# Performance work log

Hardware: AMD Instinct MI355X
Metric: run time of the kernel (lower is better)

The kernel has to match this reference:

```python
import jax, jax.numpy as jnp
import numpy as np
from jax import lax

ITER, L, D, H = 8, 4096, 512, 256


def setup_inputs() -> dict:
    key = jax.random.key(0)
    ks = jax.random.split(key, 12)
    sD = 1.0 / np.sqrt(D)
    sH = 1.0 / np.sqrt(H)
    return {
        "embeddings_seq": jax.random.normal(ks[0], (ITER, L, D), jnp.float32),
        "ROIs": jax.random.uniform(ks[1], (1, L, 3), jnp.float32),
        "Wx": jax.random.normal(ks[2], (L, D), jnp.float32) * sD,
        "bx": jax.random.normal(ks[3], (L,), jnp.float32) * 0.01,
        "Wy": jax.random.normal(ks[4], (L, D), jnp.float32) * sD,
        "by": jax.random.normal(ks[5], (L,), jnp.float32) * 0.01,
        "Wz": jax.random.normal(ks[6], (L, D), jnp.float32) * sD,
        "bz": jax.random.normal(ks[7], (L,), jnp.float32) * 0.01,
        "Ws": jax.random.normal(ks[8], (D, H), jnp.float32) * sD,
        "bs": jax.random.normal(ks[9], (H,), jnp.float32) * 0.01,
        "Wh": jax.random.normal(ks[10], (L, H), jnp.float32) * sH,
        "bh": jax.random.normal(ks[11], (L,), jnp.float32) * 0.01,
    }


def reference(embeddings_seq, ROIs, Wx, bx, Wy, by, Wz, bz, Ws, bs, Wh, bh):
    # size_tensor = [1/767, 1/767, 1/575]
    size = jnp.array([1.0 / 767, 1.0 / 767, 1.0 / 575], dtype=embeddings_seq.dtype)

    def dec(h):  # grouped Conv1d(k=D, groups=L) == per-landmark dot product; h: [L, D]
        x = jnp.sum(Wx * h, axis=-1) + bx
        y = jnp.sum(Wy * h, axis=-1) + by
        z = jnp.sum(Wz * h, axis=-1) + bz
        return jnp.stack([x, y, z], axis=-1)  # [L, 3]

    def gate_head(h):  # Linear+Tanh shared, then per-landmark grouped conv; h: [L, D]
        s = jnp.tanh(h @ Ws + bs)          # [L, H]
        return jnp.sum(Wh * s, axis=-1) + bh  # [L]

    emb0 = embeddings_seq[0]                  # [L, D]
    rois0 = ROIs[0]                           # [L, 3]
    predict0 = dec(emb0) * size + rois0       # [L, 3]

    def step(carry, emb):
        h, c, pred = carry
        rois = pred                           # previous prediction becomes new ROIs
        gf = gate_head(h)                     # [L]
        ga = gate_head(emb)                   # [L]
        g = jax.nn.softmax(jnp.stack([gf, ga], axis=-1), axis=-1)  # [L, 2]
        g0, g1 = g[:, 0:1], g[:, 1:2]
        h = h * g0 + emb * g1
        c = c * g0 + rois * g1
        pred = dec(h) * size + lax.stop_gradient(c)
        return (h, c, pred), pred

    init = (emb0, rois0, predict0)
    _, preds = lax.scan(step, init, embeddings_seq[1:])  # [ITER-1, L, 3]
    return jnp.concatenate([predict0[None], preds], axis=0)  # [ITER, L, 3]
```

## Files before the change

kernel.cpp:

```cpp
#include <hip/hip_runtime.h>
#include <stdint.h>

#define L_DIM 4096
#define D_DIM 512
#define H_DIM 256
#define T_DIM 8

typedef short bf16x8 __attribute__((ext_vector_type(8)));
typedef float f32x4 __attribute__((ext_vector_type(4)));

__device__ __forceinline__ unsigned short f2bf(float f) {
    union { float f; unsigned int u; } c; c.f = f;
    unsigned int u = c.u;
    unsigned int r = (u + 0x7fffu + ((u >> 16) & 1u)) >> 16;
    return (unsigned short)r;
}

__device__ __forceinline__ float wave_sum(float x) {
    #pragma unroll
    for (int off = 32; off > 0; off >>= 1) x += __shfl_xor(x, off, 64);
    return x;
}

__device__ __forceinline__ float dot4(float4 a, float4 b) {
    return a.x * b.x + a.y * b.y + a.z * b.z + a.w * b.w;
}

__device__ __forceinline__ float fast_tanh(float x) {
    float e = __expf(2.0f * x);
    return 1.0f - 2.0f / (e + 1.0f);
}

__global__ void k_transpose_ws(const float* __restrict__ Ws,
                               unsigned short* __restrict__ WsT) {
    int idx = blockIdx.x * 256 + threadIdx.x;
    int j = idx >> 9;
    int k = idx & 511;
    WsT[idx] = f2bf(Ws[k * H_DIM + j]);
}

__global__ __launch_bounds__(512) void k_gemm_v(const float* __restrict__ emb,
                                                const unsigned short* __restrict__ WsT,
                                                float* __restrict__ v) {
    __shared__ __align__(16) char smem[48 * 1024];
    char* As = smem;
    char* Bs = smem + 16 * 1024;

    const int tid  = threadIdx.x;
    const int lane = tid & 63;
    const int wid  = tid >> 6;
    const int wm   = wid & 1;
    const int wn   = wid >> 1;
    const long rowBase = (long)blockIdx.x * 128;

    f32x4 zero = {0.f, 0.f, 0.f, 0.f};
    f32x4 acc[4][4];
    #pragma unroll
    for (int mi = 0; mi < 4; mi++)
        #pragma unroll
        for (int ni = 0; ni < 4; ni++) acc[mi][ni] = zero;

    for (int kt = 0; kt < 8; ++kt) {
        __syncthreads();
        #pragma unroll
        for (int p = 0; p < 4; p++) {
            int g   = p * 512 + tid;
            int row = g >> 4;
            int q   = g & 15;
            float4 s = *(const float4*)(emb + (rowBase + row) * D_DIM + kt * 64 + q * 4);
            unsigned short b0 = f2bf(s.x), b1 = f2bf(s.y), b2 = f2bf(s.z), b3 = f2bf(s.w);
            uint2 pk;
            pk.x = (unsigned int)b0 | ((unsigned int)b1 << 16);
            pk.y = (unsigned int)b2 | ((unsigned int)b3 << 16);
            *(uint2*)(As + (row * 128 + ((q * 8) ^ ((row & 7) << 4)))) = pk;
        }
        #pragma unroll
        for (int p = 0; p < 4; p++) {
            int g  = p * 512 + tid;
            int j  = g >> 3;
            int ko = g & 7;
            uint4 d = *(const uint4*)(WsT + j * D_DIM + kt * 64 + ko * 8);
            *(uint4*)(Bs + (j * 128 + ((ko * 16) ^ ((j & 7) << 4)))) = d;
        }
        __syncthreads();

        #pragma unroll
        for (int ks = 0; ks < 2; ++ks) {
            bf16x8 a[4], b[4];
            #pragma unroll
            for (int mi = 0; mi < 4; mi++) {
                int row = wm * 64 + mi * 16 + (lane & 15);
                a[mi] = *(const bf16x8*)(As + (row * 128 +
                          ((ks * 64 + (lane >> 4) * 16) ^ ((row & 7) << 4))));
            }
            #pragma unroll
            for (int ni = 0; ni < 4; ni++) {
                int j = wn * 64 + ni * 16 + (lane & 15);
                b[ni] = *(const bf16x8*)(Bs + (j * 128 +
                          ((ks * 64 + (lane >> 4) * 16) ^ ((j & 7) << 4))));
            }
            #pragma unroll
            for (int mi = 0; mi < 4; mi++)
                #pragma unroll
                for (int ni = 0; ni < 4; ni++)
                    acc[mi][ni] = __builtin_amdgcn_mfma_f32_16x16x32_bf16(
                        a[mi], b[ni], acc[mi][ni], 0, 0, 0);
        }
    }

    #pragma unroll
    for (int mi = 0; mi < 4; mi++)
        #pragma unroll
        for (int ni = 0; ni < 4; ni++)
            #pragma unroll
            for (int r = 0; r < 4; r++) {
                long row = rowBase + wm * 64 + mi * 16 + (lane >> 4) * 4 + r;
                int  col = wn * 64 + ni * 16 + (lane & 15);
                v[row * H_DIM + col] = acc[mi][ni][r];
            }
}

__global__ __launch_bounds__(256) void k_seq(
    const float* __restrict__ emb, const float* __restrict__ rois,
    const float* __restrict__ Wx, const float* __restrict__ bx,
    const float* __restrict__ Wy, const float* __restrict__ by,
    const float* __restrict__ Wz, const float* __restrict__ bz,
    const float* __restrict__ bs, const float* __restrict__ Wh,
    const float* __restrict__ bh, const float* __restrict__ v,
    float* __restrict__ out) {
    const int lane = threadIdx.x & 63;
    const int l = blockIdx.x * 4 + (threadIdx.x >> 6);
    const int j4 = lane * 4;
    const int d8 = lane * 8;

    float4 Wh4 = *(const float4*)(Wh + (long)l * H_DIM + j4);
    float4 bs4 = *(const float4*)(bs + j4);
    float4 wx0 = *(const float4*)(Wx + (long)l * D_DIM + d8);
    float4 wx1 = *(const float4*)(Wx + (long)l * D_DIM + d8 + 4);
    float4 wy0 = *(const float4*)(Wy + (long)l * D_DIM + d8);
    float4 wy1 = *(const float4*)(Wy + (long)l * D_DIM + d8 + 4);
    float4 wz0 = *(const float4*)(Wz + (long)l * D_DIM + d8);
    float4 wz1 = *(const float4*)(Wz + (long)l * D_DIM + d8 + 4);
    float bxl = bx[l], byl = by[l], bzl = bz[l], bhl = bh[l];
    const float sx = 1.f / 767.f, sy = 1.f / 767.f, sz = 1.f / 575.f;

    float4 e0 = *(const float4*)(emb + (long)l * D_DIM + d8);
    float4 e1 = *(const float4*)(emb + (long)l * D_DIM + d8 + 4);
    float dx = wave_sum(dot4(wx0, e0) + dot4(wx1, e1));
    float dy = wave_sum(dot4(wy0, e0) + dot4(wy1, e1));
    float dz = wave_sum(dot4(wz0, e0) + dot4(wz1, e1));
    float4 u4 = *(const float4*)(v + (long)l * H_DIM + j4);
    float cx = rois[l * 3 + 0], cy = rois[l * 3 + 1], cz = rois[l * 3 + 2];
    float prx = (dx + bxl) * sx + cx;
    float pry = (dy + byl) * sy + cy;
    float prz = (dz + bzl) * sz + cz;
    if (lane == 0) {
        out[l * 3 + 0] = prx; out[l * 3 + 1] = pry; out[l * 3 + 2] = prz;
    }

    for (int t = 1; t < T_DIM; ++t) {
        const float* eb = emb + ((long)t * L_DIM + l) * D_DIM;
        float4 f0 = *(const float4*)(eb + d8);
        float4 f1 = *(const float4*)(eb + d8 + 4);
        float4 v4 = *(const float4*)(v + ((long)t * L_DIM + l) * H_DIM + j4);

        float pxt = wave_sum(dot4(wx0, f0) + dot4(wx1, f1));
        float pyt = wave_sum(dot4(wy0, f0) + dot4(wy1, f1));
        float pzt = wave_sum(dot4(wz0, f0) + dot4(wz1, f1));

        float4 sf, sa;
        sf.x = fast_tanh(u4.x + bs4.x); sf.y = fast_tanh(u4.y + bs4.y);
        sf.z = fast_tanh(u4.z + bs4.z); sf.w = fast_tanh(u4.w + bs4.w);
        sa.x = fast_tanh(v4.x + bs4.x); sa.y = fast_tanh(v4.y + bs4.y);
        sa.z = fast_tanh(v4.z + bs4.z); sa.w = fast_tanh(v4.w + bs4.w);
        float gf = wave_sum(dot4(Wh4, sf)) + bhl;
        float ga = wave_sum(dot4(Wh4, sa)) + bhl;

        float g0 = 1.0f / (1.0f + __expf(ga - gf));
        float g1 = 1.0f - g0;

        u4.x = g0 * u4.x + g1 * v4.x; u4.y = g0 * u4.y + g1 * v4.y;
        u4.z = g0 * u4.z + g1 * v4.z; u4.w = g0 * u4.w + g1 * v4.w;

        cx = cx * g0 + prx * g1; cy = cy * g0 + pry * g1; cz = cz * g0 + prz * g1;
        dx = g0 * dx + g1 * pxt; dy = g0 * dy + g1 * pyt; dz = g0 * dz + g1 * pzt;

        prx = (dx + bxl) * sx + cx;
        pry = (dy + byl) * sy + cy;
        prz = (dz + bzl) * sz + cz;
        if (lane == 0) {
            float* o = out + (long)t * (L_DIM * 3) + l * 3;
            o[0] = prx; o[1] = pry; o[2] = prz;
        }
    }
}

extern "C" void kernel_launch(void* const* d_in, const int* in_sizes, int n_in,
                              void* d_out, int out_size, void* d_ws, size_t ws_size,
                              hipStream_t stream) {
    const float* emb  = (const float*)d_in[0];
    const float* rois = (const float*)d_in[1];
    const float* Wx   = (const float*)d_in[2];
    const float* bx   = (const float*)d_in[3];
    const float* Wy   = (const float*)d_in[4];
    const float* by   = (const float*)d_in[5];
    const float* Wz   = (const float*)d_in[6];
    const float* bz   = (const float*)d_in[7];
    const float* Ws   = (const float*)d_in[8];
    const float* bs   = (const float*)d_in[9];
    const float* Wh   = (const float*)d_in[10];
    const float* bh   = (const float*)d_in[11];
    float* out = (float*)d_out;

    float* v = (float*)d_ws;
    unsigned short* WsT = (unsigned short*)((char*)d_ws + (size_t)32768 * 256 * 4);

    hipLaunchKernelGGL(k_transpose_ws, dim3(512), dim3(256), 0, stream, Ws, WsT);
    hipLaunchKernelGGL(k_gemm_v, dim3(256), dim3(512), 0, stream, emb, WsT, v);
    hipLaunchKernelGGL(k_seq, dim3(1024), dim3(256), 0, stream,
                       emb, rois, Wx, bx, Wy, by, Wz, bz, bs, Wh, bh, v, out);
}
```

Before: 163.9 us.

## Double-buffer GEMM tiles, store v in bf16, batch independent reductions in seq kernel

The GEMM kernel now uses 64-row tiles over 512 blocks, with double-buffered shared memory so the next K slice is fetched from global memory while MFMAs run on the current one. It writes v as bf16 instead of fp32, halving the intermediate write and read traffic. The sequential kernel now loads all timesteps up front and does their independent dot products, tanh and wave reductions before the recurrence, leaving only the forget-gate reduction on the serial path. The costs are extra rounding of v to bf16, more registers, and 80 KB of shared memory per block, which limits occupancy.

```diff
diff --git a/kernel.cpp b/kernel.cpp
--- a/kernel.cpp
+++ b/kernel.cpp
@@ -16,6 +16,19 @@
     return (unsigned short)r;
 }
 
+__device__ __forceinline__ float bits2f(unsigned int u) {
+    union { unsigned int u; float f; } c; c.u = u; return c.f;
+}
+
+__device__ __forceinline__ float4 unpack_bf4(uint2 q) {
+    float4 r;
+    r.x = bits2f(q.x << 16);
+    r.y = bits2f(q.x & 0xffff0000u);
+    r.z = bits2f(q.y << 16);
+    r.w = bits2f(q.y & 0xffff0000u);
+    return r;
+}
+
 __device__ __forceinline__ float wave_sum(float x) {
     #pragma unroll
     for (int off = 32; off > 0; off >>= 1) x += __shfl_xor(x, off, 64);
@@ -29,6 +42,13 @@
 __device__ __forceinline__ float fast_tanh(float x) {
     float e = __expf(2.0f * x);
     return 1.0f - 2.0f / (e + 1.0f);
+}
+
+__device__ __forceinline__ float4 tanh4b(float4 a, float4 b) {
+    float4 r;
+    r.x = fast_tanh(a.x + b.x); r.y = fast_tanh(a.y + b.y);
+    r.z = fast_tanh(a.z + b.z); r.w = fast_tanh(a.w + b.w);
+    return r;
 }
 
 __global__ void k_transpose_ws(const float* __restrict__ Ws,
@@ -39,84 +59,124 @@
     WsT[idx] = f2bf(Ws[k * H_DIM + j]);
 }
 
-__global__ __launch_bounds__(512) void k_gemm_v(const float* __restrict__ emb,
-                                                const unsigned short* __restrict__ WsT,
-                                                float* __restrict__ v) {
-    __shared__ __align__(16) char smem[48 * 1024];
-    char* As = smem;
-    char* Bs = smem + 16 * 1024;
+__global__ __launch_bounds__(512, 4) void k_gemm_v(
+    const float* __restrict__ emb,
+    const unsigned short* __restrict__ WsT,
+    unsigned short* __restrict__ v) {
+    __shared__ __align__(16) char smem[81920];
 
     const int tid  = threadIdx.x;
     const int lane = tid & 63;
     const int wid  = tid >> 6;
-    const int wm   = wid & 1;
-    const int wn   = wid >> 1;
-    const long rowBase = (long)blockIdx.x * 128;
-
-    f32x4 zero = {0.f, 0.f, 0.f, 0.f};
-    f32x4 acc[4][4];
-    #pragma unroll
-    for (int mi = 0; mi < 4; mi++)
-        #pragma unroll
-        for (int ni = 0; ni < 4; ni++) acc[mi][ni] = zero;
-
+    const int wm   = wid >> 2;
+    const int wn   = wid & 3;
+    const long rowBase = (long)blockIdx.x * 64;
+
+    const int arow = tid >> 4, aq = tid & 15;
+    const int bj   = tid >> 3, bko = tid & 7;
+    const float*          ag = emb + (rowBase + arow) * D_DIM + aq * 4;
+    const unsigned short* bg = WsT + (long)bj * D_DIM + bko * 8;
+
+    const int adst0 = arow * 128 + ((aq * 8) ^ ((arow & 7) << 4));
+    const int adst1 = (arow + 32) * 128 + ((aq * 8) ^ (((arow + 32) & 7) << 4));
+    const int bdst[4] = {
+        bj * 128 + ((bko * 16) ^ ((bj & 7) << 4)),
+        (bj + 64) * 128 + ((bko * 16) ^ (((bj + 64) & 7) << 4)),
+        (bj + 128) * 128 + ((bko * 16) ^ (((bj + 128) & 7) << 4)),
+        (bj + 192) * 128 + ((bko * 16) ^ (((bj + 192) & 7) << 4))};
+
+    f32x4 acc[2][4];
+    #pragma unroll
+    for (int mi = 0; mi < 2; mi++)
+        #pragma unroll
+        for (int ni = 0; ni < 4; ni++) acc[mi][ni] = (f32x4){0.f, 0.f, 0.f, 0.f};
+
+    {
+        float4 a0 = *(const float4*)(ag);
+        float4 a1 = *(const float4*)(ag + 32 * D_DIM);
+        char* As = smem;
+        char* Bs = smem + 8192;
+        uint2 p0, p1;
+        p0.x = (unsigned)f2bf(a0.x) | ((unsigned)f2bf(a0.y) << 16);
+        p0.y = (unsigned)f2bf(a0.z) | ((unsigned)f2bf(a0.w) << 16);
+        p1.x = (unsigned)f2bf(a1.x) | ((unsigned)f2bf(a1.y) << 16);
+        p1.y = (unsigned)f2bf(a1.z) | ((unsigned)f2bf(a1.w) << 16);
+        *(uint2*)(As + adst0) = p0;
+        *(uint2*)(As + adst1) = p1;
+        #pragma unroll
+        for (int p = 0; p < 4; p++)
+            *(uint4*)(Bs + bdst[p]) = *(const uint4*)(bg + (long)p * 64 * D_DIM);
+    }
+    __syncthreads();
+
+    #pragma unroll
     for (int kt = 0; kt < 8; ++kt) {
-        __syncthreads();
-        #pragma unroll
-        for (int p = 0; p < 4; p++) {
-            int g   = p * 512 + tid;
-            int row = g >> 4;
-            int q   = g & 15;
-            float4 s = *(const float4*)(emb + (rowBase + row) * D_DIM + kt * 64 + q * 4);
-            unsigned short b0 = f2bf(s.x), b1 = f2bf(s.y), b2 = f2bf(s.z), b3 = f2bf(s.w);
-            uint2 pk;
-            pk.x = (unsigned int)b0 | ((unsigned int)b1 << 16);
-            pk.y = (unsigned int)b2 | ((unsigned int)b3 << 16);
-            *(uint2*)(As + (row * 128 + ((q * 8) ^ ((row & 7) << 4)))) = pk;
-        }
-        #pragma unroll
-        for (int p = 0; p < 4; p++) {
-            int g  = p * 512 + tid;
-            int j  = g >> 3;
-            int ko = g & 7;
-            uint4 d = *(const uint4*)(WsT + j * D_DIM + kt * 64 + ko * 8);
-            *(uint4*)(Bs + (j * 128 + ((ko * 16) ^ ((j & 7) << 4)))) = d;
-        }
-        __syncthreads();
+        char* As = smem + (kt & 1) * 40960;
+        char* Bs = As + 8192;
+        char* Asn = smem + ((kt + 1) & 1) * 40960;
+        char* Bsn = Asn + 8192;
+
+        float4 a0, a1;
+        uint4 b0, b1, b2, b3;
+        if (kt < 7) {
+            const float* ap = ag + (kt + 1) * 64;
+            a0 = *(const float4*)(ap);
+            a1 = *(const float4*)(ap + 32 * D_DIM);
+            const unsigned short* bp = bg + (kt + 1) * 64;
+            b0 = *(const uint4*)(bp);
+            b1 = *(const uint4*)(bp + (long)64 * D_DIM);
+            b2 = *(const uint4*)(bp + (long)128 * D_DIM);
+            b3 = *(const uint4*)(bp + (long)192 * D_DIM);
+        }
 
         #pragma unroll
         for (int ks = 0; ks < 2; ++ks) {
-            bf16x8 a[4], b[4];
-            #pragma unroll
-            for (int mi = 0; mi < 4; mi++) {
-                int row = wm * 64 + mi * 16 + (lane & 15);
-                a[mi] = *(const bf16x8*)(As + (row * 128 +
-                          ((ks * 64 + (lane >> 4) * 16) ^ ((row & 7) << 4))));
+            bf16x8 a[2], b[4];
+            #pragma unroll
+            for (int mi = 0; mi < 2; mi++) {
+                int row = wm * 32 + mi * 16 + (lane & 15);
+                a[mi] = *(const bf16x8*)(As + row * 128 +
+                          (((ks * 64) + (lane >> 4) * 16) ^ ((row & 7) << 4)));
             }
             #pragma unroll
             for (int ni = 0; ni < 4; ni++) {
                 int j = wn * 64 + ni * 16 + (lane & 15);
-                b[ni] = *(const bf16x8*)(Bs + (j * 128 +
-                          ((ks * 64 + (lane >> 4) * 16) ^ ((j & 7) << 4))));
+                b[ni] = *(const bf16x8*)(Bs + j * 128 +
+                          (((ks * 64) + (lane >> 4) * 16) ^ ((j & 7) << 4)));
             }
             #pragma unroll
-            for (int mi = 0; mi < 4; mi++)
+            for (int mi = 0; mi < 2; mi++)
                 #pragma unroll
                 for (int ni = 0; ni < 4; ni++)
                     acc[mi][ni] = __builtin_amdgcn_mfma_f32_16x16x32_bf16(
                         a[mi], b[ni], acc[mi][ni], 0, 0, 0);
         }
-    }
-
-    #pragma unroll
-    for (int mi = 0; mi < 4; mi++)
+
+        if (kt < 7) {
+            uint2 p0, p1;
+            p0.x = (unsigned)f2bf(a0.x) | ((unsigned)f2bf(a0.y) << 16);
+            p0.y = (unsigned)f2bf(a0.z) | ((unsigned)f2bf(a0.w) << 16);
+            p1.x = (unsigned)f2bf(a1.x) | ((unsigned)f2bf(a1.y) << 16);
+            p1.y = (unsigned)f2bf(a1.z) | ((unsigned)f2bf(a1.w) << 16);
+            *(uint2*)(Asn + adst0) = p0;
+            *(uint2*)(Asn + adst1) = p1;
+            *(uint4*)(Bsn + bdst[0]) = b0;
+            *(uint4*)(Bsn + bdst[1]) = b1;
+            *(uint4*)(Bsn + bdst[2]) = b2;
+            *(uint4*)(Bsn + bdst[3]) = b3;
+        }
+        __syncthreads();
+    }
+
+    #pragma unroll
+    for (int mi = 0; mi < 2; mi++)
         #pragma unroll
         for (int ni = 0; ni < 4; ni++)
             #pragma unroll
             for (int r = 0; r < 4; r++) {
-                long row = rowBase + wm * 64 + mi * 16 + (lane >> 4) * 4 + r;
+                long row = rowBase + wm * 32 + mi * 16 + (lane >> 4) * 4 + r;
                 int  col = wn * 64 + ni * 16 + (lane & 15);
-                v[row * H_DIM + col] = acc[mi][ni][r];
+                v[row * H_DIM + col] = f2bf(acc[mi][ni][r]);
             }
 }
 
@@ -126,7 +186,7 @@
     const float* __restrict__ Wy, const float* __restrict__ by,
     const float* __restrict__ Wz, const float* __restrict__ bz,
     const float* __restrict__ bs, const float* __restrict__ Wh,
-    const float* __restrict__ bh, const float* __restrict__ v,
+    const float* __restrict__ bh, const unsigned short* __restrict__ v,
     float* __restrict__ out) {
     const int lane = threadIdx.x & 63;
     const int l = blockIdx.x * 4 + (threadIdx.x >> 6);
@@ -144,13 +204,32 @@
     float bxl = bx[l], byl = by[l], bzl = bz[l], bhl = bh[l];
     const float sx = 1.f / 767.f, sy = 1.f / 767.f, sz = 1.f / 575.f;
 
-    float4 e0 = *(const float4*)(emb + (long)l * D_DIM + d8);
-    float4 e1 = *(const float4*)(emb + (long)l * D_DIM + d8 + 4);
-    float dx = wave_sum(dot4(wx0, e0) + dot4(wx1, e1));
-    float dy = wave_sum(dot4(wy0, e0) + dot4(wy1, e1));
-    float dz = wave_sum(dot4(wz0, e0) + dot4(wz1, e1));
-    float4 u4 = *(const float4*)(v + (long)l * H_DIM + j4);
+    float px[T_DIM], py[T_DIM], pz[T_DIM], ga[T_DIM];
+    uint2 vvp[T_DIM];
+    #pragma unroll
+    for (int t = 0; t < T_DIM; ++t) {
+        const float* eb = emb + ((long)t * L_DIM + l) * D_DIM + d8;
+        float4 f0 = *(const float4*)(eb);
+        float4 f1 = *(const float4*)(eb + 4);
+        px[t] = dot4(wx0, f0) + dot4(wx1, f1);
+        py[t] = dot4(wy0, f0) + dot4(wy1, f1);
+        pz[t] = dot4(wz0, f0) + dot4(wz1, f1);
+        uint2 q = *(const uint2*)(v + ((long)t * L_DIM + l) * H_DIM + j4);
+        vvp[t] = q;
+        float4 sa = tanh4b(unpack_bf4(q), bs4);
+        ga[t] = dot4(Wh4, sa);
+    }
+    #pragma unroll
+    for (int t = 0; t < T_DIM; ++t) {
+        px[t] = wave_sum(px[t]);
+        py[t] = wave_sum(py[t]);
+        pz[t] = wave_sum(pz[t]);
+        ga[t] = wave_sum(ga[t]) + bhl;
+    }
+
+    float4 u4 = unpack_bf4(vvp[0]);
     float cx = rois[l * 3 + 0], cy = rois[l * 3 + 1], cz = rois[l * 3 + 2];
+    float dx = px[0], dy = py[0], dz = pz[0];
     float prx = (dx + bxl) * sx + cx;
     float pry = (dy + byl) * sy + cy;
     float prz = (dz + bzl) * sz + cz;
@@ -158,32 +237,20 @@
         out[l * 3 + 0] = prx; out[l * 3 + 1] = pry; out[l * 3 + 2] = prz;
     }
 
+    #pragma unroll
     for (int t = 1; t < T_DIM; ++t) {
-        const float* eb = emb + ((long)t * L_DIM + l) * D_DIM;
-        float4 f0 = *(const float4*)(eb + d8);
-        float4 f1 = *(const float4*)(eb + d8 + 4);
-        float4 v4 = *(const float4*)(v + ((long)t * L_DIM + l) * H_DIM + j4);
-
-        float pxt = wave_sum(dot4(wx0, f0) + dot4(wx1, f1));
-        float pyt = wave_sum(dot4(wy0, f0) + dot4(wy1, f1));
-        float pzt = wave_sum(dot4(wz0, f0) + dot4(wz1, f1));
-
-        float4 sf, sa;
-        sf.x = fast_tanh(u4.x + bs4.x); sf.y = fast_tanh(u4.y + bs4.y);
-        sf.z = fast_tanh(u4.z + bs4.z); sf.w = fast_tanh(u4.w + bs4.w);
-        sa.x = fast_tanh(v4.x + bs4.x); sa.y = fast_tanh(v4.y + bs4.y);
-        sa.z = fast_tanh(v4.z + bs4.z); sa.w = fast_tanh(v4.w + bs4.w);
+        float4 sf = tanh4b(u4, bs4);
         float gf = wave_sum(dot4(Wh4, sf)) + bhl;
-        float ga = wave_sum(dot4(Wh4, sa)) + bhl;
-
-        float g0 = 1.0f / (1.0f + __expf(ga - gf));
+
+        float g0 = 1.0f / (1.0f + __expf(ga[t] - gf));
         float g1 = 1.0f - g0;
 
+        float4 v4 = unpack_bf4(vvp[t]);
         u4.x = g0 * u4.x + g1 * v4.x; u4.y = g0 * u4.y + g1 * v4.y;
         u4.z = g0 * u4.z + g1 * v4.z; u4.w = g0 * u4.w + g1 * v4.w;
 
         cx = cx * g0 + prx * g1; cy = cy * g0 + pry * g1; cz = cz * g0 + prz * g1;
-        dx = g0 * dx + g1 * pxt; dy = g0 * dy + g1 * pyt; dz = g0 * dz + g1 * pzt;
+        dx = g0 * dx + g1 * px[t]; dy = g0 * dy + g1 * py[t]; dz = g0 * dz + g1 * pz[t];
 
         prx = (dx + bxl) * sx + cx;
         pry = (dy + byl) * sy + cy;
@@ -212,11 +279,11 @@
     const float* bh   = (const float*)d_in[11];
     float* out = (float*)d_out;
 
-    float* v = (float*)d_ws;
-    unsigned short* WsT = (unsigned short*)((char*)d_ws + (size_t)32768 * 256 * 4);
+    unsigned short* v   = (unsigned short*)d_ws;
+    unsigned short* WsT = (unsigned short*)((char*)d_ws + (size_t)16 * 1024 * 1024);
 
     hipLaunchKernelGGL(k_transpose_ws, dim3(512), dim3(256), 0, stream, Ws, WsT);
-    hipLaunchKernelGGL(k_gemm_v, dim3(256), dim3(512), 0, stream, emb, WsT, v);
+    hipLaunchKernelGGL(k_gemm_v, dim3(512), dim3(512), 0, stream, emb, WsT, v);
     hipLaunchKernelGGL(k_seq, dim3(1024), dim3(256), 0, stream,
                        emb, rois, Wx, bx, Wy, by, Wz, bz, bs, Wh, bh, v, out);
 }
```

New measurement: 167.0 us. About the same (+1.9%).
